# Kernel tuning notes

Measured on AMD Instinct MI355X. Metric: run time of the kernel, lower is better.

The kernel has to match this reference:

```python
import jax, jax.numpy as jnp
import numpy as np

B, S, DM, H = 16, 512, 256, 8
DF = DM // H          # per-head feature dim
K_INDEX = 5           # keep top-(K_INDEX) probs per row (SparseKT soft-threshold top-k)
NEG_MASK = -1e32      # fill for causal mask
NEG_SPARSE = -1e16    # fill for sub-threshold probs before re-softmax


def setup_inputs() -> dict:
    key = jax.random.key(0)
    ks = jax.random.split(key, 6)
    sc = 1.0 / np.sqrt(DM)  # ~xavier scale
    q = jax.random.normal(ks[0], (B, S, DM), jnp.float32)
    k = jax.random.normal(ks[1], (B, S, DM), jnp.float32)
    v = jax.random.normal(ks[2], (B, S, DM), jnp.float32)
    # causal lower-triangular mask, [1,1,S,S]; scores where mask==0 -> -1e32
    mask = jnp.tril(jnp.ones((S, S), jnp.int32))[None, None]
    # k_linear / v_linear / out_proj weights (key_query_same=True -> q shares k_linear)
    Wk = jax.random.normal(ks[3], (DM, DM), jnp.float32) * sc
    Wv = jax.random.normal(ks[4], (DM, DM), jnp.float32) * sc
    Wo = jax.random.normal(ks[5], (DM, DM), jnp.float32) * sc
    bk = jnp.zeros((DM,), jnp.float32)
    bv = jnp.zeros((DM,), jnp.float32)
    bo = jnp.zeros((DM,), jnp.float32)
    return {"q": q, "k": k, "v": v, "mask": mask, "zero_pad": 1,
            "Wk": Wk, "bk": bk, "Wv": Wv, "bv": bv, "Wo": Wo, "bo": bo}


def _heads(x, W, b):
    # Linear then split heads: [B,S,DM] -> [B,H,S,DF]
    y = x @ W.T + b
    return y.reshape(B, S, H, DF).transpose(0, 2, 1, 3)


def reference(q, k, v, mask, zero_pad, Wk, bk, Wv, bv, Wo, bo):
    qh = _heads(q, Wk, bk)  # key_query_same: q uses k_linear
    kh = _heads(k, Wk, bk)
    vh = _heads(v, Wv, bv)

    scores = jnp.einsum("bhqd,bhkd->bhqk", qh, kh) / np.sqrt(DF)
    scores = jnp.where(mask == 0, jnp.float32(NEG_MASK), scores)
    attn = jax.nn.softmax(scores, axis=-1)

    if K_INDEX + 1 < S:
        attn_a = attn[:, :, : K_INDEX + 1, :]          # short rows kept as-is
        attn_b = attn[:, :, K_INDEX + 1 :, :]          # rows to sparsify
        # threshold = K_INDEX-th largest prob per row (== sorted desc [k_index-1])
        thr = jax.lax.top_k(attn_b, K_INDEX)[0][..., -1:]
        attn_b = jnp.where(attn_b - thr >= 0, attn_b, jnp.float32(NEG_SPARSE))
        attn_b = jax.nn.softmax(attn_b, axis=-1)
        attn = jnp.concatenate([attn_a, attn_b], axis=2)

    if zero_pad:
        attn = jnp.concatenate(
            [jnp.zeros_like(attn[:, :, :1, :]), attn[:, :, 1:, :]], axis=2)

    # dropout is identity in eval mode
    ctx = jnp.einsum("bhqk,bhkd->bhqd", attn, vh)
    concat = ctx.transpose(0, 2, 1, 3).reshape(B, S, DM)
    output = concat @ Wo.T + bo
    return output, attn
```

## Files before the change

kernel.cpp:

```cpp
#include <hip/hip_runtime.h>
#include <hip/hip_bf16.h>
#include <math.h>

#define BB 16
#define SS 512
#define DMM 256
#define HH 8
#define DFF 32
#define KIDX 5

template<int TM, bool HEADS>
__device__ __forceinline__ void gemm_body(
    const float* __restrict__ X, const float* __restrict__ W,
    const float* __restrict__ bias, float* __restrict__ Y)
{
  constexpr int RM = TM / 16;
  constexpr int NA = TM / 32;
  __shared__ float As[32][TM];
  __shared__ float Bs[32][64];
  const int tid = threadIdx.x;
  const int tx = tid & 15;
  const int ty = tid >> 4;
  const int m0 = blockIdx.x * TM;
  const int n0 = blockIdx.y * 64;

  float4 pa[NA], pb[2];
  #pragma unroll
  for (int i = 0; i < NA; ++i) {
    const int f = tid * NA + i;
    pa[i] = *reinterpret_cast<const float4*>(&X[(size_t)(m0 + (f >> 3)) * DMM + ((f & 7) << 2)]);
  }
  #pragma unroll
  for (int i = 0; i < 2; ++i) {
    const int f = tid * 2 + i;
    pb[i] = *reinterpret_cast<const float4*>(&W[(size_t)(n0 + (f >> 3)) * DMM + ((f & 7) << 2)]);
  }

  float acc[RM][4] = {};

  for (int k0 = 0; k0 < DMM; k0 += 32) {
    #pragma unroll
    for (int i = 0; i < NA; ++i) {
      const int f = tid * NA + i;
      const int ar = f >> 3, ac4 = (f & 7) << 2;
      As[ac4 + 0][ar] = pa[i].x; As[ac4 + 1][ar] = pa[i].y;
      As[ac4 + 2][ar] = pa[i].z; As[ac4 + 3][ar] = pa[i].w;
    }
    #pragma unroll
    for (int i = 0; i < 2; ++i) {
      const int f = tid * 2 + i;
      const int br = f >> 3, bc4 = (f & 7) << 2;
      Bs[bc4 + 0][br] = pb[i].x; Bs[bc4 + 1][br] = pb[i].y;
      Bs[bc4 + 2][br] = pb[i].z; Bs[bc4 + 3][br] = pb[i].w;
    }
    __syncthreads();
    if (k0 + 32 < DMM) {
      #pragma unroll
      for (int i = 0; i < NA; ++i) {
        const int f = tid * NA + i;
        pa[i] = *reinterpret_cast<const float4*>(&X[(size_t)(m0 + (f >> 3)) * DMM + k0 + 32 + ((f & 7) << 2)]);
      }
      #pragma unroll
      for (int i = 0; i < 2; ++i) {
        const int f = tid * 2 + i;
        pb[i] = *reinterpret_cast<const float4*>(&W[(size_t)(n0 + (f >> 3)) * DMM + k0 + 32 + ((f & 7) << 2)]);
      }
    }
    #pragma unroll
    for (int kk = 0; kk < 32; ++kk) {
      const float4 b4 = *reinterpret_cast<const float4*>(&Bs[kk][tx * 4]);
      #pragma unroll
      for (int r4 = 0; r4 < RM / 4; ++r4) {
        const float4 a4 = *reinterpret_cast<const float4*>(&As[kk][ty * RM + r4 * 4]);
        const int i0 = r4 * 4;
        acc[i0+0][0] += a4.x * b4.x; acc[i0+0][1] += a4.x * b4.y; acc[i0+0][2] += a4.x * b4.z; acc[i0+0][3] += a4.x * b4.w;
        acc[i0+1][0] += a4.y * b4.x; acc[i0+1][1] += a4.y * b4.y; acc[i0+1][2] += a4.y * b4.z; acc[i0+1][3] += a4.y * b4.w;
        acc[i0+2][0] += a4.z * b4.x; acc[i0+2][1] += a4.z * b4.y; acc[i0+2][2] += a4.z * b4.z; acc[i0+2][3] += a4.z * b4.w;
        acc[i0+3][0] += a4.w * b4.x; acc[i0+3][1] += a4.w * b4.y; acc[i0+3][2] += a4.w * b4.z; acc[i0+3][3] += a4.w * b4.w;
      }
    }
    __syncthreads();
  }

  const int n = n0 + tx * 4;
  const float4 b4 = *reinterpret_cast<const float4*>(&bias[n]);
  #pragma unroll
  for (int i = 0; i < RM; ++i) {
    const int m = m0 + ty * RM + i;
    float4 o;
    o.x = acc[i][0] + b4.x; o.y = acc[i][1] + b4.y;
    o.z = acc[i][2] + b4.z; o.w = acc[i][3] + b4.w;
    if (HEADS) {
      const int b = m >> 9;
      const int s = m & (SS - 1);
      const int h = n >> 5;
      const int d = n & (DFF - 1);
      *reinterpret_cast<float4*>(&Y[(((size_t)b * HH + h) * SS + s) * DFF + d]) = o;
    } else {
      *reinterpret_cast<float4*>(&Y[(size_t)m * DMM + n]) = o;
    }
  }
}

__global__ __launch_bounds__(256) void proj_kernel(
    const float* __restrict__ q, const float* __restrict__ k, const float* __restrict__ v,
    const float* __restrict__ Wk, const float* __restrict__ bk,
    const float* __restrict__ Wv, const float* __restrict__ bv,
    float* __restrict__ qh, float* __restrict__ kh, float* __restrict__ vh)
{
  const int z = blockIdx.z;
  const float* X = (z == 0) ? q : (z == 1) ? k : v;
  const float* W = (z == 2) ? Wv : Wk;
  const float* bias = (z == 2) ? bv : bk;
  float* Y = (z == 0) ? qh : (z == 1) ? kh : vh;
  gemm_body<128, true>(X, W, bias, Y);
}

__global__ __launch_bounds__(256) void out_kernel(
    const float* __restrict__ X, const float* __restrict__ Wo,
    const float* __restrict__ bo, float* __restrict__ Y)
{
  gemm_body<64, false>(X, Wo, bo, Y);
}

__global__ __launch_bounds__(256) void attn_kernel(
    const float* __restrict__ qh,
    const float* __restrict__ kh,
    const float* __restrict__ vh,
    const int* __restrict__ zp,
    float* __restrict__ attn,
    float* __restrict__ concat)
{
  __shared__ float4 Ksh[64 * 8];
  __shared__ float ws_w[4][8];
  __shared__ int   ws_c[4][8];

  const int tid  = threadIdx.x;
  const int lane = tid & 63;
  const int wave = tid >> 6;
  const int grp  = blockIdx.x;
  const int bh   = grp >> 7;
  const int base = (grp & 127) << 2;
  const int qrow = base + wave;
  const int b    = bh >> 3;
  const int h    = bh & 7;
  const int ncols = qrow + 1;
  const float scale = 0.17677669529663688f;

  const float* kb = kh + (size_t)bh * SS * DFF;
  const float* vb = vh + (size_t)bh * SS * DFF;

  float4 q4[8];
  {
    const float* qp = qh + ((size_t)bh * SS + qrow) * DFF;
    #pragma unroll
    for (int g = 0; g < 8; ++g)
      q4[g] = *reinterpret_cast<const float4*>(qp + g * 4);
  }

  const int nch  = ((base + 3) >> 6) + 1;
  const int mych = qrow >> 6;

  const int scol = tid & 63;
  const int g0   = (tid >> 6) << 1;

  float p[8];
  #pragma unroll
  for (int i = 0; i < 8; ++i) p[i] = -INFINITY;

  const float* kp0 = kb + (size_t)scol * DFF + g0 * 4;
  float4 r0 = *reinterpret_cast<const float4*>(kp0);
  float4 r1 = *reinterpret_cast<const float4*>(kp0 + 4);

  for (int c = 0; c < nch; ++c) {
    Ksh[(scol << 3) + ((g0 + scol) & 7)]     = r0;
    Ksh[(scol << 3) + ((g0 + 1 + scol) & 7)] = r1;
    __syncthreads();
    if (c + 1 < nch) {
      const float* kp = kb + (size_t)(((c + 1) << 6) + scol) * DFF + g0 * 4;
      r0 = *reinterpret_cast<const float4*>(kp);
      r1 = *reinterpret_cast<const float4*>(kp + 4);
    }
    if (c <= mych) {
      const int col = (c << 6) + lane;
      float d0 = 0.f, d1 = 0.f;
      #pragma unroll
      for (int g = 0; g < 8; ++g) {
        const int pg = (g + lane) & 7;
        const float4 kv = Ksh[(lane << 3) + pg];
        const float4 qv = q4[g];
        d0 = fmaf(qv.x, kv.x, d0);
        d1 = fmaf(qv.y, kv.y, d1);
        d0 = fmaf(qv.z, kv.z, d0);
        d1 = fmaf(qv.w, kv.w, d1);
      }
      if (col < ncols) p[c] = (d0 + d1) * scale;
    }
    __syncthreads();
  }

  float m = p[0];
  #pragma unroll
  for (int s2 = 1; s2 < 8; ++s2) m = fmaxf(m, p[s2]);
  #pragma unroll
  for (int off = 32; off >= 1; off >>= 1) m = fmaxf(m, __shfl_xor(m, off, 64));
  float sum = 0.f;
  #pragma unroll
  for (int s2 = 0; s2 < 8; ++s2) {
    const float e = (p[s2] == -INFINITY) ? 0.f : __expf(p[s2] - m);
    p[s2] = e;
    sum += e;
  }
  #pragma unroll
  for (int off = 32; off >= 1; off >>= 1) sum += __shfl_xor(sum, off, 64);
  const float inv = 1.0f / sum;
  #pragma unroll
  for (int s2 = 0; s2 < 8; ++s2) p[s2] *= inv;

  float neww[8];
  if (qrow > KIDX) {
    float v[8];
    #pragma unroll
    for (int s2 = 0; s2 < 8; ++s2) {
      const int col = lane + (s2 << 6);
      v[s2] = (col < ncols) ? p[s2] : -INFINITY;
    }
    #define CE(i, j) { const float t = fmaxf(v[i], v[j]); v[j] = fminf(v[i], v[j]); v[i] = t; }
    CE(0,1) CE(2,3) CE(4,5) CE(6,7)
    CE(0,2) CE(1,3) CE(4,6) CE(5,7)
    CE(1,2) CE(5,6)
    CE(0,4) CE(1,5) CE(2,6) CE(3,7)
    CE(2,4) CE(3,5)
    CE(1,2) CE(3,4) CE(5,6)
    #undef CE
    float a0 = v[0], a1 = v[1], a2 = v[2], a3 = v[3], a4 = v[4];
    #pragma unroll
    for (int off = 1; off <= 32; off <<= 1) {
      const float b0 = __shfl_xor(a0, off, 64);
      const float b1 = __shfl_xor(a1, off, 64);
      const float b2 = __shfl_xor(a2, off, 64);
      const float b3 = __shfl_xor(a3, off, 64);
      const float b4 = __shfl_xor(a4, off, 64);
      const float n0 = fmaxf(a0, b0);
      const float n1 = fmaxf(fmaxf(a1, b1), fminf(a0, b0));
      const float n2 = fmaxf(fmaxf(a2, b2), fmaxf(fminf(a0, b1), fminf(a1, b0)));
      const float n3 = fmaxf(fmaxf(a3, b3),
                       fmaxf(fmaxf(fminf(a0, b2), fminf(a1, b1)), fminf(a2, b0)));
      const float n4 = fmaxf(fmaxf(a4, b4),
                       fmaxf(fmaxf(fminf(a0, b3), fminf(a1, b2)),
                             fmaxf(fminf(a2, b1), fminf(a3, b0))));
      a0 = n0; a1 = n1; a2 = n2; a3 = n3; a4 = n4;
    }
    const float m1 = a0;
    const float thr = a4;
    float nsum = 0.f;
    #pragma unroll
    for (int s2 = 0; s2 < 8; ++s2) {
      const int col = lane + (s2 << 6);
      float e = 0.f;
      if (col < ncols && (p[s2] - thr >= 0.f)) e = __expf(p[s2] - m1);
      neww[s2] = e;
      nsum += e;
    }
    #pragma unroll
    for (int off = 32; off >= 1; off >>= 1) nsum += __shfl_xor(nsum, off, 64);
    const float ninv = 1.0f / nsum;
    #pragma unroll
    for (int s2 = 0; s2 < 8; ++s2) neww[s2] *= ninv;
  } else {
    #pragma unroll
    for (int s2 = 0; s2 < 8; ++s2) neww[s2] = p[s2];
  }

  if (qrow == 0 && *zp != 0) {
    #pragma unroll
    for (int s2 = 0; s2 < 8; ++s2) neww[s2] = 0.f;
  }

  {
    float* arow = attn + ((size_t)bh * SS + qrow) * SS;
    #pragma unroll
    for (int s2 = 0; s2 < 8; ++s2) arow[lane + (s2 << 6)] = neww[s2];
  }

  {
    unsigned long long msks[8];
    #pragma unroll
    for (int s2 = 0; s2 < 8; ++s2) msks[s2] = __ballot(neww[s2] != 0.f);
    int rbase = 0;
    #pragma unroll
    for (int s2 = 0; s2 < 8; ++s2) {
      const unsigned long long msk = msks[s2];
      const int myr = rbase + __popcll(msk & ((1ull << lane) - 1ull));
      if (((msk >> lane) & 1ull) && myr < 8) {
        ws_w[wave][myr] = neww[s2];
        ws_c[wave][myr] = (s2 << 6) | lane;
      }
      rbase += __popcll(msk);
    }
    const int nk = rbase;
    if (lane < 8 && lane >= nk) { ws_w[wave][lane] = 0.f; ws_c[wave][lane] = 0; }

    const int dd = lane & 31;
    float accv = 0.f;
    if (nk <= 8) {
      #pragma unroll
      for (int i = 0; i < 8; ++i)
        accv += ws_w[wave][i] * vb[(size_t)ws_c[wave][i] * DFF + dd];
    } else {
      #pragma unroll
      for (int s2 = 0; s2 < 8; ++s2) {
        unsigned long long msk = msks[s2];
        while (msk) {
          const int src = __ffsll(msk) - 1;
          msk &= msk - 1;
          accv += __shfl(neww[s2], src, 64) * vb[(size_t)(src + (s2 << 6)) * DFF + dd];
        }
      }
    }
    if (lane < 32)
      concat[((size_t)b * SS + qrow) * DMM + h * DFF + dd] = accv;
  }
}

extern "C" void kernel_launch(void* const* d_in, const int* in_sizes, int n_in,
                              void* d_out, int out_size, void* d_ws, size_t ws_size,
                              hipStream_t stream) {
  const float* q  = (const float*)d_in[0];
  const float* k  = (const float*)d_in[1];
  const float* v  = (const float*)d_in[2];
  const int*   zp = (const int*)d_in[4];
  const float* Wk = (const float*)d_in[5];
  const float* bk = (const float*)d_in[6];
  const float* Wv = (const float*)d_in[7];
  const float* bv = (const float*)d_in[8];
  const float* Wo = (const float*)d_in[9];
  const float* bo = (const float*)d_in[10];

  float* ws     = (float*)d_ws;
  float* qhp    = ws;
  float* khp    = ws + 2097152;
  float* vhp    = ws + 4194304;
  float* concat = ws + 6291456;

  float* outp  = (float*)d_out;
  float* attnp = outp + (size_t)BB * SS * DMM;

  proj_kernel<<<dim3(64, 4, 3), 256, 0, stream>>>(q, k, v, Wk, bk, Wv, bv, qhp, khp, vhp);
  attn_kernel<<<dim3(BB * HH * SS / 4), 256, 0, stream>>>(qhp, khp, vhp, zp, attnp, concat);
  out_kernel<<<dim3(128, 4), 256, 0, stream>>>(concat, Wo, bo, outp);
}
```

Baseline: 333.7 us.

## Process two query rows per wave in attention and retile GEMMs with 2x2 register subtiles

The attention kernel now gives each wave two query rows (r and r+4), so every K tile staged in shared memory feeds twice the dot products and the grid is halved. The per-row softmax, top-k and PV tail moves into a shared device function that is called once per row. The projection and output GEMMs switch to a K-step of 16 with larger N tiles and 2x2 strided 4x4 register subtiles, giving more reuse per shared-memory load. The cost is higher register pressure, which may lower occupancy, and fewer blocks in flight.

```diff
diff --git a/kernel.cpp b/kernel.cpp
--- a/kernel.cpp
+++ b/kernel.cpp
@@ -9,95 +9,114 @@
 #define DFF 32
 #define KIDX 5
 
-template<int TM, bool HEADS>
+template<int TM, int TN, int GM, int GN, bool HEADS>
 __device__ __forceinline__ void gemm_body(
     const float* __restrict__ X, const float* __restrict__ W,
     const float* __restrict__ bias, float* __restrict__ Y)
 {
-  constexpr int RM = TM / 16;
-  constexpr int NA = TM / 32;
-  __shared__ float As[32][TM];
-  __shared__ float Bs[32][64];
+  __shared__ float As[16][TM];
+  __shared__ float Bs[16][TN];
+  constexpr int NA = TM / 64;
+  constexpr int NB = TN / 64;
   const int tid = threadIdx.x;
   const int tx = tid & 15;
   const int ty = tid >> 4;
   const int m0 = blockIdx.x * TM;
-  const int n0 = blockIdx.y * 64;
-
-  float4 pa[NA], pb[2];
+  const int n0 = blockIdx.y * TN;
+
+  float4 pa[NA], pb[NB];
   #pragma unroll
   for (int i = 0; i < NA; ++i) {
     const int f = tid * NA + i;
-    pa[i] = *reinterpret_cast<const float4*>(&X[(size_t)(m0 + (f >> 3)) * DMM + ((f & 7) << 2)]);
-  }
-  #pragma unroll
-  for (int i = 0; i < 2; ++i) {
-    const int f = tid * 2 + i;
-    pb[i] = *reinterpret_cast<const float4*>(&W[(size_t)(n0 + (f >> 3)) * DMM + ((f & 7) << 2)]);
-  }
-
-  float acc[RM][4] = {};
-
-  for (int k0 = 0; k0 < DMM; k0 += 32) {
+    pa[i] = *reinterpret_cast<const float4*>(&X[(size_t)(m0 + (f >> 2)) * DMM + ((f & 3) << 2)]);
+  }
+  #pragma unroll
+  for (int i = 0; i < NB; ++i) {
+    const int f = tid * NB + i;
+    pb[i] = *reinterpret_cast<const float4*>(&W[(size_t)(n0 + (f >> 2)) * DMM + ((f & 3) << 2)]);
+  }
+
+  float acc[GM * 4][GN * 4] = {};
+
+  for (int k0 = 0; k0 < DMM; k0 += 16) {
     #pragma unroll
     for (int i = 0; i < NA; ++i) {
       const int f = tid * NA + i;
-      const int ar = f >> 3, ac4 = (f & 7) << 2;
-      As[ac4 + 0][ar] = pa[i].x; As[ac4 + 1][ar] = pa[i].y;
-      As[ac4 + 2][ar] = pa[i].z; As[ac4 + 3][ar] = pa[i].w;
-    }
-    #pragma unroll
-    for (int i = 0; i < 2; ++i) {
-      const int f = tid * 2 + i;
-      const int br = f >> 3, bc4 = (f & 7) << 2;
-      Bs[bc4 + 0][br] = pb[i].x; Bs[bc4 + 1][br] = pb[i].y;
-      Bs[bc4 + 2][br] = pb[i].z; Bs[bc4 + 3][br] = pb[i].w;
+      const int r = f >> 2, c4 = (f & 3) << 2;
+      As[c4 + 0][r] = pa[i].x; As[c4 + 1][r] = pa[i].y;
+      As[c4 + 2][r] = pa[i].z; As[c4 + 3][r] = pa[i].w;
+    }
+    #pragma unroll
+    for (int i = 0; i < NB; ++i) {
+      const int f = tid * NB + i;
+      const int r = f >> 2, c4 = (f & 3) << 2;
+      Bs[c4 + 0][r] = pb[i].x; Bs[c4 + 1][r] = pb[i].y;
+      Bs[c4 + 2][r] = pb[i].z; Bs[c4 + 3][r] = pb[i].w;
     }
     __syncthreads();
-    if (k0 + 32 < DMM) {
+    if (k0 + 16 < DMM) {
       #pragma unroll
       for (int i = 0; i < NA; ++i) {
         const int f = tid * NA + i;
-        pa[i] = *reinterpret_cast<const float4*>(&X[(size_t)(m0 + (f >> 3)) * DMM + k0 + 32 + ((f & 7) << 2)]);
-      }
-      #pragma unroll
-      for (int i = 0; i < 2; ++i) {
-        const int f = tid * 2 + i;
-        pb[i] = *reinterpret_cast<const float4*>(&W[(size_t)(n0 + (f >> 3)) * DMM + k0 + 32 + ((f & 7) << 2)]);
-      }
-    }
-    #pragma unroll
-    for (int kk = 0; kk < 32; ++kk) {
-      const float4 b4 = *reinterpret_cast<const float4*>(&Bs[kk][tx * 4]);
-      #pragma unroll
-      for (int r4 = 0; r4 < RM / 4; ++r4) {
-        const float4 a4 = *reinterpret_cast<const float4*>(&As[kk][ty * RM + r4 * 4]);
-        const int i0 = r4 * 4;
-        acc[i0+0][0] += a4.x * b4.x; acc[i0+0][1] += a4.x * b4.y; acc[i0+0][2] += a4.x * b4.z; acc[i0+0][3] += a4.x * b4.w;
-        acc[i0+1][0] += a4.y * b4.x; acc[i0+1][1] += a4.y * b4.y; acc[i0+1][2] += a4.y * b4.z; acc[i0+1][3] += a4.y * b4.w;
-        acc[i0+2][0] += a4.z * b4.x; acc[i0+2][1] += a4.z * b4.y; acc[i0+2][2] += a4.z * b4.z; acc[i0+2][3] += a4.z * b4.w;
-        acc[i0+3][0] += a4.w * b4.x; acc[i0+3][1] += a4.w * b4.y; acc[i0+3][2] += a4.w * b4.z; acc[i0+3][3] += a4.w * b4.w;
+        pa[i] = *reinterpret_cast<const float4*>(&X[(size_t)(m0 + (f >> 2)) * DMM + k0 + 16 + ((f & 3) << 2)]);
+      }
+      #pragma unroll
+      for (int i = 0; i < NB; ++i) {
+        const int f = tid * NB + i;
+        pb[i] = *reinterpret_cast<const float4*>(&W[(size_t)(n0 + (f >> 2)) * DMM + k0 + 16 + ((f & 3) << 2)]);
+      }
+    }
+    #pragma unroll
+    for (int kk = 0; kk < 16; ++kk) {
+      float4 af[GM], bf[GN];
+      #pragma unroll
+      for (int gm = 0; gm < GM; ++gm)
+        af[gm] = *reinterpret_cast<const float4*>(&As[kk][gm * (TM / 2) + ty * 4]);
+      #pragma unroll
+      for (int gn = 0; gn < GN; ++gn)
+        bf[gn] = *reinterpret_cast<const float4*>(&Bs[kk][gn * (TN / 2) + tx * 4]);
+      #pragma unroll
+      for (int gm = 0; gm < GM; ++gm) {
+        const float am[4] = {af[gm].x, af[gm].y, af[gm].z, af[gm].w};
+        #pragma unroll
+        for (int i = 0; i < 4; ++i) {
+          #pragma unroll
+          for (int gn = 0; gn < GN; ++gn) {
+            acc[gm*4+i][gn*4+0] = fmaf(am[i], bf[gn].x, acc[gm*4+i][gn*4+0]);
+            acc[gm*4+i][gn*4+1] = fmaf(am[i], bf[gn].y, acc[gm*4+i][gn*4+1]);
+            acc[gm*4+i][gn*4+2] = fmaf(am[i], bf[gn].z, acc[gm*4+i][gn*4+2]);
+            acc[gm*4+i][gn*4+3] = fmaf(am[i], bf[gn].w, acc[gm*4+i][gn*4+3]);
+          }
+        }
       }
     }
     __syncthreads();
   }
 
-  const int n = n0 + tx * 4;
-  const float4 b4 = *reinterpret_cast<const float4*>(&bias[n]);
-  #pragma unroll
-  for (int i = 0; i < RM; ++i) {
-    const int m = m0 + ty * RM + i;
-    float4 o;
-    o.x = acc[i][0] + b4.x; o.y = acc[i][1] + b4.y;
-    o.z = acc[i][2] + b4.z; o.w = acc[i][3] + b4.w;
-    if (HEADS) {
-      const int b = m >> 9;
-      const int s = m & (SS - 1);
-      const int h = n >> 5;
-      const int d = n & (DFF - 1);
-      *reinterpret_cast<float4*>(&Y[(((size_t)b * HH + h) * SS + s) * DFF + d]) = o;
-    } else {
-      *reinterpret_cast<float4*>(&Y[(size_t)m * DMM + n]) = o;
+  #pragma unroll
+  for (int gn = 0; gn < GN; ++gn) {
+    const int n = n0 + gn * (TN / 2) + tx * 4;
+    const float4 b4 = *reinterpret_cast<const float4*>(&bias[n]);
+    #pragma unroll
+    for (int gm = 0; gm < GM; ++gm) {
+      #pragma unroll
+      for (int i = 0; i < 4; ++i) {
+        const int m = m0 + gm * (TM / 2) + ty * 4 + i;
+        float4 o;
+        o.x = acc[gm*4+i][gn*4+0] + b4.x;
+        o.y = acc[gm*4+i][gn*4+1] + b4.y;
+        o.z = acc[gm*4+i][gn*4+2] + b4.z;
+        o.w = acc[gm*4+i][gn*4+3] + b4.w;
+        if (HEADS) {
+          const int bb = m >> 9;
+          const int s  = m & (SS - 1);
+          const int hh = n >> 5;
+          const int d  = n & (DFF - 1);
+          *reinterpret_cast<float4*>(&Y[(((size_t)bb * HH + hh) * SS + s) * DFF + d]) = o;
+        } else {
+          *reinterpret_cast<float4*>(&Y[(size_t)m * DMM + n]) = o;
+        }
+      }
     }
   }
 }
@@ -113,91 +132,25 @@
   const float* W = (z == 2) ? Wv : Wk;
   const float* bias = (z == 2) ? bv : bk;
   float* Y = (z == 0) ? qh : (z == 1) ? kh : vh;
-  gemm_body<128, true>(X, W, bias, Y);
+  gemm_body<128, 128, 2, 2, true>(X, W, bias, Y);
 }
 
 __global__ __launch_bounds__(256) void out_kernel(
     const float* __restrict__ X, const float* __restrict__ Wo,
     const float* __restrict__ bo, float* __restrict__ Y)
 {
-  gemm_body<64, false>(X, Wo, bo, Y);
-}
-
-__global__ __launch_bounds__(256) void attn_kernel(
-    const float* __restrict__ qh,
-    const float* __restrict__ kh,
-    const float* __restrict__ vh,
+  gemm_body<128, 64, 2, 1, false>(X, Wo, bo, Y);
+}
+
+__device__ __forceinline__ void attn_row_tail(
+    float* p, const int qrow, const int lane,
+    const int b, const int h, const int bh,
     const int* __restrict__ zp,
-    float* __restrict__ attn,
-    float* __restrict__ concat)
-{
-  __shared__ float4 Ksh[64 * 8];
-  __shared__ float ws_w[4][8];
-  __shared__ int   ws_c[4][8];
-
-  const int tid  = threadIdx.x;
-  const int lane = tid & 63;
-  const int wave = tid >> 6;
-  const int grp  = blockIdx.x;
-  const int bh   = grp >> 7;
-  const int base = (grp & 127) << 2;
-  const int qrow = base + wave;
-  const int b    = bh >> 3;
-  const int h    = bh & 7;
+    float* __restrict__ attn, float* __restrict__ concat,
+    const float* __restrict__ vb,
+    float* wsw, int* wsc)
+{
   const int ncols = qrow + 1;
-  const float scale = 0.17677669529663688f;
-
-  const float* kb = kh + (size_t)bh * SS * DFF;
-  const float* vb = vh + (size_t)bh * SS * DFF;
-
-  float4 q4[8];
-  {
-    const float* qp = qh + ((size_t)bh * SS + qrow) * DFF;
-    #pragma unroll
-    for (int g = 0; g < 8; ++g)
-      q4[g] = *reinterpret_cast<const float4*>(qp + g * 4);
-  }
-
-  const int nch  = ((base + 3) >> 6) + 1;
-  const int mych = qrow >> 6;
-
-  const int scol = tid & 63;
-  const int g0   = (tid >> 6) << 1;
-
-  float p[8];
-  #pragma unroll
-  for (int i = 0; i < 8; ++i) p[i] = -INFINITY;
-
-  const float* kp0 = kb + (size_t)scol * DFF + g0 * 4;
-  float4 r0 = *reinterpret_cast<const float4*>(kp0);
-  float4 r1 = *reinterpret_cast<const float4*>(kp0 + 4);
-
-  for (int c = 0; c < nch; ++c) {
-    Ksh[(scol << 3) + ((g0 + scol) & 7)]     = r0;
-    Ksh[(scol << 3) + ((g0 + 1 + scol) & 7)] = r1;
-    __syncthreads();
-    if (c + 1 < nch) {
-      const float* kp = kb + (size_t)(((c + 1) << 6) + scol) * DFF + g0 * 4;
-      r0 = *reinterpret_cast<const float4*>(kp);
-      r1 = *reinterpret_cast<const float4*>(kp + 4);
-    }
-    if (c <= mych) {
-      const int col = (c << 6) + lane;
-      float d0 = 0.f, d1 = 0.f;
-      #pragma unroll
-      for (int g = 0; g < 8; ++g) {
-        const int pg = (g + lane) & 7;
-        const float4 kv = Ksh[(lane << 3) + pg];
-        const float4 qv = q4[g];
-        d0 = fmaf(qv.x, kv.x, d0);
-        d1 = fmaf(qv.y, kv.y, d1);
-        d0 = fmaf(qv.z, kv.z, d0);
-        d1 = fmaf(qv.w, kv.w, d1);
-      }
-      if (col < ncols) p[c] = (d0 + d1) * scale;
-    }
-    __syncthreads();
-  }
 
   float m = p[0];
   #pragma unroll
@@ -293,20 +246,20 @@
       const unsigned long long msk = msks[s2];
       const int myr = rbase + __popcll(msk & ((1ull << lane) - 1ull));
       if (((msk >> lane) & 1ull) && myr < 8) {
-        ws_w[wave][myr] = neww[s2];
-        ws_c[wave][myr] = (s2 << 6) | lane;
+        wsw[myr] = neww[s2];
+        wsc[myr] = (s2 << 6) | lane;
       }
       rbase += __popcll(msk);
     }
     const int nk = rbase;
-    if (lane < 8 && lane >= nk) { ws_w[wave][lane] = 0.f; ws_c[wave][lane] = 0; }
+    if (lane < 8 && lane >= nk) { wsw[lane] = 0.f; wsc[lane] = 0; }
 
     const int dd = lane & 31;
     float accv = 0.f;
     if (nk <= 8) {
       #pragma unroll
       for (int i = 0; i < 8; ++i)
-        accv += ws_w[wave][i] * vb[(size_t)ws_c[wave][i] * DFF + dd];
+        accv += wsw[i] * vb[(size_t)wsc[i] * DFF + dd];
     } else {
       #pragma unroll
       for (int s2 = 0; s2 < 8; ++s2) {
@@ -321,6 +274,93 @@
     if (lane < 32)
       concat[((size_t)b * SS + qrow) * DMM + h * DFF + dd] = accv;
   }
+}
+
+__global__ __launch_bounds__(256) void attn_kernel(
+    const float* __restrict__ qh,
+    const float* __restrict__ kh,
+    const float* __restrict__ vh,
+    const int* __restrict__ zp,
+    float* __restrict__ attn,
+    float* __restrict__ concat)
+{
+  __shared__ float4 Ksh[64 * 8];
+  __shared__ float ws_w[4][8];
+  __shared__ int   ws_c[4][8];
+
+  const int tid  = threadIdx.x;
+  const int lane = tid & 63;
+  const int wave = tid >> 6;
+  const int grp  = blockIdx.x;
+  const int bh   = grp >> 6;
+  const int base = (grp & 63) << 3;
+  const int rA   = base + wave;
+  const int rB   = rA + 4;
+  const int b    = bh >> 3;
+  const int h    = bh & 7;
+  const float scale = 0.17677669529663688f;
+
+  const float* kb = kh + (size_t)bh * SS * DFF;
+  const float* vb = vh + (size_t)bh * SS * DFF;
+
+  float4 qA[8], qB[8];
+  {
+    const float* qpA = qh + ((size_t)bh * SS + rA) * DFF;
+    const float* qpB = qh + ((size_t)bh * SS + rB) * DFF;
+    #pragma unroll
+    for (int g = 0; g < 8; ++g) {
+      qA[g] = *reinterpret_cast<const float4*>(qpA + g * 4);
+      qB[g] = *reinterpret_cast<const float4*>(qpB + g * 4);
+    }
+  }
+
+  const int nch = (base >> 6) + 1;
+
+  const int scol = tid & 63;
+  const int g0   = (tid >> 6) << 1;
+
+  float pA[8], pB[8];
+  #pragma unroll
+  for (int i = 0; i < 8; ++i) { pA[i] = -INFINITY; pB[i] = -INFINITY; }
+
+  const float* kp0 = kb + (size_t)scol * DFF + g0 * 4;
+  float4 r0 = *reinterpret_cast<const float4*>(kp0);
+  float4 r1 = *reinterpret_cast<const float4*>(kp0 + 4);
+
+  for (int c = 0; c < nch; ++c) {
+    Ksh[(scol << 3) + ((g0 + scol) & 7)]     = r0;
+    Ksh[(scol << 3) + ((g0 + 1 + scol) & 7)] = r1;
+    __syncthreads();
+    if (c + 1 < nch) {
+      const float* kp = kb + (size_t)(((c + 1) << 6) + scol) * DFF + g0 * 4;
+      r0 = *reinterpret_cast<const float4*>(kp);
+      r1 = *reinterpret_cast<const float4*>(kp + 4);
+    }
+    {
+      const int col = (c << 6) + lane;
+      float d0A = 0.f, d1A = 0.f, d0B = 0.f, d1B = 0.f;
+      #pragma unroll
+      for (int g = 0; g < 8; ++g) {
+        const float4 kv = Ksh[(lane << 3) + ((g + lane) & 7)];
+        const float4 qa = qA[g];
+        const float4 qb = qB[g];
+        d0A = fmaf(qa.x, kv.x, d0A);
+        d1A = fmaf(qa.y, kv.y, d1A);
+        d0A = fmaf(qa.z, kv.z, d0A);
+        d1A = fmaf(qa.w, kv.w, d1A);
+        d0B = fmaf(qb.x, kv.x, d0B);
+        d1B = fmaf(qb.y, kv.y, d1B);
+        d0B = fmaf(qb.z, kv.z, d0B);
+        d1B = fmaf(qb.w, kv.w, d1B);
+      }
+      if (col <= rA) pA[c] = (d0A + d1A) * scale;
+      if (col <= rB) pB[c] = (d0B + d1B) * scale;
+    }
+    __syncthreads();
+  }
+
+  attn_row_tail(pA, rA, lane, b, h, bh, zp, attn, concat, vb, ws_w[wave], ws_c[wave]);
+  attn_row_tail(pB, rB, lane, b, h, bh, zp, attn, concat, vb, ws_w[wave], ws_c[wave]);
 }
 
 extern "C" void kernel_launch(void* const* d_in, const int* in_sizes, int n_in,
@@ -346,7 +386,7 @@
   float* outp  = (float*)d_out;
   float* attnp = outp + (size_t)BB * SS * DMM;
 
-  proj_kernel<<<dim3(64, 4, 3), 256, 0, stream>>>(q, k, v, Wk, bk, Wv, bv, qhp, khp, vhp);
-  attn_kernel<<<dim3(BB * HH * SS / 4), 256, 0, stream>>>(qhp, khp, vhp, zp, attnp, concat);
-  out_kernel<<<dim3(128, 4), 256, 0, stream>>>(concat, Wo, bo, outp);
-}
+  proj_kernel<<<dim3(64, 2, 3), 256, 0, stream>>>(q, k, v, Wk, bk, Wv, bv, qhp, khp, vhp);
+  attn_kernel<<<dim3(BB * HH * SS / 8), 256, 0, stream>>>(qhp, khp, vhp, zp, attnp, concat);
+  out_kernel<<<dim3(64, 4), 256, 0, stream>>>(concat, Wo, bo, outp);
+}
```

Result: faster. 324.9 us (-2.6%).
